# Kernel optimization log

Measured on AMD Instinct MI355X. Metric: run time of the kernel, lower is better.

## Reference

```python
import jax, jax.numpy as jnp
import numpy as np

D_MODEL = 1024
N_HEAD = 16
T = 2048
HEAD = D_MODEL // N_HEAD  # 64
RANKS = [32, 16, 8, 8]
BLOCKS = [2048, 1024, 512, 256]  # seq_len // 2**i ('default')
OFFS = np.cumsum([0] + RANKS)


def setup_inputs() -> dict:
    key = jax.random.key(0)
    k0, k1, k2 = jax.random.split(key, 3)
    s = 0.02
    x = jax.random.normal(k0, (1, T, D_MODEL), dtype=jnp.float32)
    W_attn = jax.random.normal(k1, (D_MODEL, 3 * D_MODEL), dtype=jnp.float32) * s
    b_attn = jnp.zeros((3 * D_MODEL,), dtype=jnp.float32)
    W_proj = jax.random.normal(k2, (D_MODEL, D_MODEL), dtype=jnp.float32) * s
    b_proj = jnp.zeros((D_MODEL,), dtype=jnp.float32)
    return {"x": x, "W_attn": W_attn, "b_attn": b_attn, "W_proj": W_proj, "b_proj": b_proj}


def reference(x, W_attn, b_attn, W_proj, b_proj):
    B = x.shape[0]
    qkv = x @ W_attn + b_attn  # (B,T,3*D)
    q, k, v = jnp.split(qkv, 3, axis=-1)
    # (B,H,T,HEAD)
    q = q.reshape(B, T, N_HEAD, HEAD).transpose(0, 2, 1, 3)
    k = k.reshape(B, T, N_HEAD, HEAD).transpose(0, 2, 1, 3)
    v = v.reshape(B, T, N_HEAD, HEAD).transpose(0, 2, 1, 3)

    att = jnp.zeros((B, N_HEAD, T, T), dtype=x.dtype)
    for i, (bdx, r) in enumerate(zip(BLOCKS, RANKS)):
        nb = T // bdx
        qi = q[..., OFFS[i]:OFFS[i + 1]].reshape(B, N_HEAD, nb, bdx, r)
        ki = k[..., OFFS[i]:OFFS[i + 1]].reshape(B, N_HEAD, nb, bdx, r)
        blk = jnp.einsum('bhnir,bhnjr->bhnij', qi, ki) * (1.0 / r)  # (B,H,nb,bdx,bdx)
        # scatter block-diagonal scores into full T x T matrix
        att5 = att.reshape(B, N_HEAD, nb, bdx, nb, bdx)
        ar = jnp.arange(nb)
        att5 = att5.at[:, :, ar, :, ar, :].add(jnp.moveaxis(blk, 2, 0))
        att = att5.reshape(B, N_HEAD, T, T)

    causal = jnp.tril(jnp.ones((T, T), dtype=bool))
    att = jnp.where(causal, att, -jnp.inf)
    att = jax.nn.softmax(att, axis=-1)
    y = att @ v  # (B,H,T,HEAD)
    y = y.transpose(0, 2, 1, 3).reshape(B, T, D_MODEL)
    return y @ W_proj + b_proj
```

## Files before the change

kernel.cpp:

```cpp
#include <hip/hip_runtime.h>

using bf16x8 = __attribute__((ext_vector_type(8))) short;
using f32x4  = __attribute__((ext_vector_type(4))) float;

#define DEVI __device__ __forceinline__

DEVI unsigned short f2bf(float f) {
  union { float ff; unsigned u; } v; v.ff = f;
  unsigned r = v.u + 0x7FFFu + ((v.u >> 16) & 1u);
  return (unsigned short)(r >> 16);
}

DEVI int cvtpk(float lo, float hi) {
  int r;
  asm("v_cvt_pk_bf16_f32 %0, %1, %2" : "=v"(r) : "v"(lo), "v"(hi));
  return r;
}

DEVI void g2l16(const void* g, void* l) {
  __builtin_amdgcn_global_load_lds(
      (const __attribute__((address_space(1))) unsigned int*)g,
      (__attribute__((address_space(3))) unsigned int*)l, 16, 0, 0);
}

__global__ void k_convx(const float* __restrict__ in, unsigned short* __restrict__ out, int n4) {
  int i = blockIdx.x * 256 + threadIdx.x;
  if (i >= n4) return;
  float4 v = reinterpret_cast<const float4*>(in)[i];
  ushort4 o;
  o.x = f2bf(v.x); o.y = f2bf(v.y); o.z = f2bf(v.z); o.w = f2bf(v.w);
  reinterpret_cast<ushort4*>(out)[i] = o;
}

__global__ void k_tconv(const float* __restrict__ in, unsigned short* __restrict__ out, int R, int C) {
  __shared__ float tile[32][33];
  int c0 = blockIdx.x * 32, r0 = blockIdx.y * 32;
  int x = threadIdx.x, y = threadIdx.y;
  for (int i = y; i < 32; i += 8) tile[i][x] = in[(size_t)(r0 + i) * C + c0 + x];
  __syncthreads();
  for (int i = y; i < 32; i += 8) out[(size_t)(c0 + i) * R + r0 + x] = f2bf(tile[x][i]);
}

__global__ __launch_bounds__(256) void k_gemm_qkv(
    const unsigned short* __restrict__ A, const unsigned short* __restrict__ Bt,
    const float* __restrict__ bias,
    unsigned short* __restrict__ qs, unsigned short* __restrict__ kbuf,
    unsigned short* __restrict__ vT) {
  constexpr int K = 1024;
  __shared__ __align__(16) unsigned short As[2][128 * 64];
  __shared__ __align__(16) unsigned short Bs[2][64 * 64];
  const int lane = threadIdx.x & 63, wid = threadIdx.x >> 6;
  const int m0 = blockIdx.y * 128, n0 = blockIdx.x * 64;
  const int wr = (wid >> 1) * 64, wc = (wid & 1) * 32;
  const int g = lane >> 4, li = lane & 15;
  f32x4 acc[4][2] = {};

#define STAGE_QKV(buf, k0)                                                              \
  {                                                                                     \
    _Pragma("unroll")                                                                   \
    for (int c = wid * 4; c < wid * 4 + 4; c++) {                                       \
      const int flat = c * 1024 + lane * 16;                                            \
      const int row = flat >> 7, colb = flat & 127;                                     \
      g2l16((const char*)A + ((size_t)(m0 + row) * K + (k0)) * 2 + colb,                \
            (char*)As[buf] + c * 1024);                                                 \
    }                                                                                   \
    _Pragma("unroll")                                                                   \
    for (int c = wid * 2; c < wid * 2 + 2; c++) {                                       \
      const int flat = c * 1024 + lane * 16;                                            \
      const int row = flat >> 7, colb = flat & 127;                                     \
      g2l16((const char*)Bt + ((size_t)(n0 + row) * K + (k0)) * 2 + colb,               \
            (char*)Bs[buf] + c * 1024);                                                 \
    }                                                                                   \
  }

  STAGE_QKV(0, 0);
  __syncthreads();
  int buf = 0;
  for (int t = 0; t < 16; t++) {
    if (t < 15) STAGE_QKV(buf ^ 1, (t + 1) * 64);
#pragma unroll
    for (int ks = 0; ks < 2; ks++) {
      const int kk = ks * 32 + g * 8;
      bf16x8 a[4], b[2];
#pragma unroll
      for (int i = 0; i < 4; i++)
        a[i] = *reinterpret_cast<const bf16x8*>(As[buf] + (wr + i * 16 + li) * 64 + kk);
#pragma unroll
      for (int j = 0; j < 2; j++)
        b[j] = *reinterpret_cast<const bf16x8*>(Bs[buf] + (wc + j * 16 + li) * 64 + kk);
#pragma unroll
      for (int i = 0; i < 4; i++)
#pragma unroll
        for (int j = 0; j < 2; j++)
          acc[i][j] = __builtin_amdgcn_mfma_f32_16x16x32_bf16(a[i], b[j], acc[i][j], 0, 0, 0);
    }
    __syncthreads();
    buf ^= 1;
  }

  const int rb = m0 + wr + g * 4;
  const int cb = n0 + wc + li;
#pragma unroll
  for (int j = 0; j < 2; j++) {
    const int c = cb + j * 16;
    const float bv = bias[c];
    const int hq = c >> 6, d = c & 63;
    const float sc = d < 32 ? 0.03125f : (d < 48 ? 0.0625f : 0.125f);
#pragma unroll
    for (int i = 0; i < 4; i++) {
#pragma unroll
      for (int r = 0; r < 4; r++) {
        const int t = rb + i * 16 + r;
        const float val = acc[i][j][r] + bv;
        if (c < 1024) {
          qs[((size_t)(hq * 2048 + t) << 6) + d] = f2bf(val * sc);
        } else if (c < 2048) {
          kbuf[((size_t)((hq - 16) * 2048 + t) << 6) + d] = f2bf(val);
        } else {
          vT[(size_t)((hq - 32) * 64 + d) * 2048 + t] = f2bf(val);
        }
      }
    }
  }
#undef STAGE_QKV
}

DEVI int chunk_off(int qt) {
  const int off[17] = {0,1,2,3,4,6,8,10,12,15,18,21,24,28,32,36,40};
  return off[qt];
}

__global__ __launch_bounds__(256) void k_attn_part(
    const unsigned short* __restrict__ qs, const unsigned short* __restrict__ kbuf,
    const unsigned short* __restrict__ vT,
    float* __restrict__ o_part, float* __restrict__ ml) {
  __shared__ __align__(16) unsigned short Ks[128 * 64];
  __shared__ __align__(16) unsigned short Vs[64 * 128];
  const int lane = threadIdx.x & 63, wid = threadIdx.x >> 6;
  const int g = lane >> 4, li = lane & 15;

  const int h = blockIdx.x / 40;
  const int rem = blockIdx.x % 40;
  int qt = 0;
#pragma unroll
  for (int i = 0; i < 16; i++)
    if (rem >= chunk_off(i + 1)) qt = i + 1;
  const int ci = rem - chunk_off(qt);
  const int kt0 = ci * 4;
  const int kt1 = min(qt, kt0 + 3);
  const int q0 = qt * 128;

  const bf16x8 bzero = {0, 0, 0, 0, 0, 0, 0, 0};

  bf16x8 qf[2][2];
#pragma unroll
  for (int mi = 0; mi < 2; mi++)
#pragma unroll
    for (int ks = 0; ks < 2; ks++) {
      const int t = q0 + wid * 32 + mi * 16 + li;
      const int d = ks * 32 + g * 8;
      qf[mi][ks] = *reinterpret_cast<const bf16x8*>(qs + ((size_t)(h * 2048 + t) << 6) + d);
    }

  f32x4 o[2][4] = {};
  float m_run[2] = {-1e30f, -1e30f}, l_run[2] = {0.f, 0.f};

  const int q256 = qt >> 1;
  for (int kt = kt0; kt <= kt1; kt++) {
    __syncthreads();
    for (int c = wid; c < 16; c += 4) {
      const int fb = c * 1024;
      const int flat = fb + lane * 16;
      {
        const int row = flat >> 7;
        const int cs = (((flat >> 4) & 7) ^ (row & 7)) << 4;
        g2l16((const char*)kbuf + (((size_t)(h * 2048 + kt * 128 + row)) << 7) + cs,
              (char*)Ks + fb);
      }
      {
        const int row = flat >> 8;
        const int cs = (((flat >> 4) & 15) ^ (row & 15)) << 4;
        g2l16((const char*)vT + ((size_t)(h * 64 + row) * 2048 + kt * 128) * 2 + cs,
              (char*)Vs + fb);
      }
    }
    __syncthreads();

    const int x = q256 ^ (kt >> 1);
    const int Keff = (x == 0) ? 64 : ((x >= 4) ? 32 : ((x >= 2) ? 48 : 56));

    f32x4 st[8][2] = {};
#pragma unroll
    for (int cf = 0; cf < 8; cf++) {
      const int krow = cf * 16 + li;
      const bf16x8 a0 = *reinterpret_cast<const bf16x8*>(
          Ks + krow * 64 + ((g ^ (krow & 7)) << 3));
      st[cf][0] = __builtin_amdgcn_mfma_f32_16x16x32_bf16(a0, qf[0][0], st[cf][0], 0, 0, 0);
      st[cf][1] = __builtin_amdgcn_mfma_f32_16x16x32_bf16(a0, qf[1][0], st[cf][1], 0, 0, 0);
    }
    if (Keff > 32) {
      const bool zf = (32 + g * 8) >= Keff;
#pragma unroll
      for (int cf = 0; cf < 8; cf++) {
        const int krow = cf * 16 + li;
        bf16x8 a1 = *reinterpret_cast<const bf16x8*>(
            Ks + krow * 64 + (((4 + g) ^ (krow & 7)) << 3));
        if (zf) a1 = bzero;
        st[cf][0] = __builtin_amdgcn_mfma_f32_16x16x32_bf16(a1, qf[0][1], st[cf][0], 0, 0, 0);
        st[cf][1] = __builtin_amdgcn_mfma_f32_16x16x32_bf16(a1, qf[1][1], st[cf][1], 0, 0, 0);
      }
    }

    if (kt == qt) {
#pragma unroll
      for (int cf = 0; cf < 8; cf++)
#pragma unroll
        for (int mi = 0; mi < 2; mi++)
#pragma unroll
          for (int r = 0; r < 4; r++) {
            const int t2 = cf * 16 + g * 4 + r;
            const int qq = wid * 32 + mi * 16 + li;
            if (t2 > qq) st[cf][mi][r] = -1e30f;
          }
    }

    int pk[2][8][2];
    float corrb[2][4];
#pragma unroll
    for (int mi = 0; mi < 2; mi++) {
      float tm = st[0][mi][0];
#pragma unroll
      for (int cf = 0; cf < 8; cf++)
#pragma unroll
        for (int r = 0; r < 4; r++)
          if (cf | r) tm = fmaxf(tm, st[cf][mi][r]);
      tm = fmaxf(tm, __shfl_xor(tm, 16));
      tm = fmaxf(tm, __shfl_xor(tm, 32));
      const float mn = fmaxf(m_run[mi], tm);
      const float corr = __expf(m_run[mi] - mn);
      m_run[mi] = mn;
      float sum = 0.f;
#pragma unroll
      for (int cf = 0; cf < 8; cf++) {
        const float p0 = __expf(st[cf][mi][0] - mn);
        const float p1 = __expf(st[cf][mi][1] - mn);
        const float p2 = __expf(st[cf][mi][2] - mn);
        const float p3 = __expf(st[cf][mi][3] - mn);
        sum += (p0 + p1) + (p2 + p3);
        pk[mi][cf][0] = cvtpk(p0, p1);
        pk[mi][cf][1] = cvtpk(p2, p3);
      }
      sum += __shfl_xor(sum, 16);
      sum += __shfl_xor(sum, 32);
      l_run[mi] = l_run[mi] * corr + sum;
      corrb[mi][0] = __shfl(corr, 4 * g + 0);
      corrb[mi][1] = __shfl(corr, 4 * g + 1);
      corrb[mi][2] = __shfl(corr, 4 * g + 2);
      corrb[mi][3] = __shfl(corr, 4 * g + 3);
    }
#pragma unroll
    for (int mi = 0; mi < 2; mi++)
#pragma unroll
      for (int nf = 0; nf < 4; nf++)
#pragma unroll
        for (int r = 0; r < 4; r++)
          o[mi][nf][r] *= corrb[mi][r];

#pragma unroll
    for (int ks2 = 0; ks2 < 4; ks2++) {
      bf16x8 pa[2];
#pragma unroll
      for (int mi = 0; mi < 2; mi++) {
        union { int i[4]; bf16x8 v; } u;
        u.i[0] = pk[mi][2 * ks2][0];
        u.i[1] = pk[mi][2 * ks2][1];
        u.i[2] = pk[mi][2 * ks2 + 1][0];
        u.i[3] = pk[mi][2 * ks2 + 1][1];
        pa[mi] = u.v;
      }
      bf16x8 vb[4];
#pragma unroll
      for (int nf = 0; nf < 4; nf++) {
        const int vrow = nf * 16 + li;
        const int rm = vrow & 15;
        const int ch0 = 4 * ks2 + (g >> 1);
        const int b8 = (g & 1) * 8;
        union { struct { int2 lo, hi; } p; bf16x8 v; } u;
        u.p.lo = *reinterpret_cast<const int2*>(
            (const char*)Vs + vrow * 256 + (((ch0 + 0) ^ rm) << 4) + b8);
        u.p.hi = *reinterpret_cast<const int2*>(
            (const char*)Vs + vrow * 256 + (((ch0 + 2) ^ rm) << 4) + b8);
        vb[nf] = u.v;
      }
#pragma unroll
      for (int mi = 0; mi < 2; mi++)
#pragma unroll
        for (int nf = 0; nf < 4; nf++)
          o[mi][nf] = __builtin_amdgcn_mfma_f32_16x16x32_bf16(pa[mi], vb[nf], o[mi][nf], 0, 0, 0);
    }
  }

  const size_t pbase = (size_t)blockIdx.x * 8192;
#pragma unroll
  for (int mi = 0; mi < 2; mi++) {
#pragma unroll
    for (int nf = 0; nf < 4; nf++)
#pragma unroll
      for (int r = 0; r < 4; r++) {
        const int row = wid * 32 + mi * 16 + g * 4 + r;
        o_part[pbase + (size_t)row * 64 + nf * 16 + li] = o[mi][nf][r];
      }
  }
  if (g == 0) {
#pragma unroll
    for (int mi = 0; mi < 2; mi++) {
      const int row = wid * 32 + mi * 16 + li;
      ml[(size_t)blockIdx.x * 256 + row] = m_run[mi];
      ml[(size_t)blockIdx.x * 256 + 128 + row] = l_run[mi];
    }
  }
}

__global__ __launch_bounds__(256) void k_combine(
    const float* __restrict__ o_part, const float* __restrict__ ml,
    unsigned short* __restrict__ yb) {
  const int h = blockIdx.x >> 4, qt = blockIdx.x & 15;
  const int nc = (qt >> 2) + 1;
  const int base = h * 40 + chunk_off(qt);
  const int row = threadIdx.x >> 1;
  const int c0 = (threadIdx.x & 1) * 32;

  float m_i[4], l_i[4];
  float M = -1e30f;
  for (int ci = 0; ci < nc; ci++) {
    m_i[ci] = ml[(size_t)(base + ci) * 256 + row];
    l_i[ci] = ml[(size_t)(base + ci) * 256 + 128 + row];
    M = fmaxf(M, m_i[ci]);
  }
  float L = 0.f, w[4];
  for (int ci = 0; ci < nc; ci++) {
    w[ci] = __expf(m_i[ci] - M);
    L += w[ci] * l_i[ci];
  }
  const float inv = 1.0f / L;

  float acc[32];
#pragma unroll
  for (int j = 0; j < 32; j++) acc[j] = 0.f;
  for (int ci = 0; ci < nc; ci++) {
    const float* src = o_part + (size_t)(base + ci) * 8192 + (size_t)row * 64 + c0;
    const float wc = w[ci];
#pragma unroll
    for (int j4 = 0; j4 < 8; j4++) {
      float4 v = reinterpret_cast<const float4*>(src)[j4];
      acc[j4 * 4 + 0] += wc * v.x;
      acc[j4 * 4 + 1] += wc * v.y;
      acc[j4 * 4 + 2] += wc * v.z;
      acc[j4 * 4 + 3] += wc * v.w;
    }
  }
  const int t = qt * 128 + row;
  unsigned short* dst = yb + (size_t)t * 1024 + h * 64 + c0;
#pragma unroll
  for (int j8 = 0; j8 < 4; j8++) {
    ushort4 pk;
    pk.x = f2bf(acc[j8 * 8 + 0] * inv);
    pk.y = f2bf(acc[j8 * 8 + 1] * inv);
    pk.z = f2bf(acc[j8 * 8 + 2] * inv);
    pk.w = f2bf(acc[j8 * 8 + 3] * inv);
    ushort4 pk2;
    pk2.x = f2bf(acc[j8 * 8 + 4] * inv);
    pk2.y = f2bf(acc[j8 * 8 + 5] * inv);
    pk2.z = f2bf(acc[j8 * 8 + 6] * inv);
    pk2.w = f2bf(acc[j8 * 8 + 7] * inv);
    reinterpret_cast<ushort4*>(dst)[j8 * 2 + 0] = pk;
    reinterpret_cast<ushort4*>(dst)[j8 * 2 + 1] = pk2;
  }
}

__global__ __launch_bounds__(256) void k_gemm_proj(
    const unsigned short* __restrict__ A, const unsigned short* __restrict__ Bt,
    const float* __restrict__ bias, float* __restrict__ out) {
  constexpr int K = 1024;
  __shared__ __align__(16) unsigned short As[2][64 * 64];
  __shared__ __align__(16) unsigned short Bs[2][64 * 64];
  const int lane = threadIdx.x & 63, wid = threadIdx.x >> 6;
  const int m0 = blockIdx.y * 64, n0 = blockIdx.x * 64;
  const int wr = (wid >> 1) * 32, wc = (wid & 1) * 32;
  const int g = lane >> 4, li = lane & 15;
  f32x4 acc[2][2] = {};

#define STAGE_PROJ(buf, k0)                                                             \
  {                                                                                     \
    _Pragma("unroll")                                                                   \
    for (int c = wid * 2; c < wid * 2 + 2; c++) {                                       \
      const int flat = c * 1024 + lane * 16;                                            \
      const int row = flat >> 7, colb = flat & 127;                                     \
      g2l16((const char*)A + ((size_t)(m0 + row) * K + (k0)) * 2 + colb,                \
            (char*)As[buf] + c * 1024);                                                 \
      g2l16((const char*)Bt + ((size_t)(n0 + row) * K + (k0)) * 2 + colb,               \
            (char*)Bs[buf] + c * 1024);                                                 \
    }                                                                                   \
  }

  STAGE_PROJ(0, 0);
  __syncthreads();
  int buf = 0;
  for (int t = 0; t < 16; t++) {
    if (t < 15) STAGE_PROJ(buf ^ 1, (t + 1) * 64);
#pragma unroll
    for (int ks = 0; ks < 2; ks++) {
      const int kk = ks * 32 + g * 8;
      bf16x8 a[2], b[2];
#pragma unroll
      for (int i = 0; i < 2; i++)
        a[i] = *reinterpret_cast<const bf16x8*>(As[buf] + (wr + i * 16 + li) * 64 + kk);
#pragma unroll
      for (int j = 0; j < 2; j++)
        b[j] = *reinterpret_cast<const bf16x8*>(Bs[buf] + (wc + j * 16 + li) * 64 + kk);
#pragma unroll
      for (int i = 0; i < 2; i++)
#pragma unroll
        for (int j = 0; j < 2; j++)
          acc[i][j] = __builtin_amdgcn_mfma_f32_16x16x32_bf16(a[i], b[j], acc[i][j], 0, 0, 0);
    }
    __syncthreads();
    buf ^= 1;
  }

  const int rb = m0 + wr + g * 4;
  const int cb = n0 + wc + li;
#pragma unroll
  for (int j = 0; j < 2; j++) {
    const int c = cb + j * 16;
    const float bv = bias[c];
#pragma unroll
    for (int i = 0; i < 2; i++) {
#pragma unroll
      for (int r = 0; r < 4; r++) {
        const int t = rb + i * 16 + r;
        out[(size_t)t * 1024 + c] = acc[i][j][r] + bv;
      }
    }
  }
#undef STAGE_PROJ
}

extern "C" void kernel_launch(void* const* d_in, const int* in_sizes, int n_in,
                              void* d_out, int out_size, void* d_ws, size_t ws_size,
                              hipStream_t stream) {
  const float* x      = (const float*)d_in[0];
  const float* W_attn = (const float*)d_in[1];
  const float* b_attn = (const float*)d_in[2];
  const float* W_proj = (const float*)d_in[3];
  const float* b_proj = (const float*)d_in[4];
  float* out = (float*)d_out;
  char* ws = (char*)d_ws;
  const size_t MB = 1024 * 1024;
  unsigned short* xb  = (unsigned short*)(ws + 0 * MB);
  unsigned short* WaT = (unsigned short*)(ws + 4 * MB);
  unsigned short* WpT = (unsigned short*)(ws + 10 * MB);
  unsigned short* qs  = (unsigned short*)(ws + 12 * MB);
  unsigned short* kb  = (unsigned short*)(ws + 16 * MB);
  unsigned short* vT  = (unsigned short*)(ws + 20 * MB);
  unsigned short* yb  = (unsigned short*)(ws + 24 * MB);
  float* o_part = (float*)(ws + 28 * MB);
  float* ml     = (float*)(ws + 48 * MB + 256 * 1024);

  k_convx<<<dim3(2048), dim3(256), 0, stream>>>(x, xb, 524288);
  k_tconv<<<dim3(96, 32), dim3(32, 8), 0, stream>>>(W_attn, WaT, 1024, 3072);
  k_tconv<<<dim3(32, 32), dim3(32, 8), 0, stream>>>(W_proj, WpT, 1024, 1024);
  k_gemm_qkv<<<dim3(48, 16), dim3(256), 0, stream>>>(xb, WaT, b_attn, qs, kb, vT);
  k_attn_part<<<dim3(640), dim3(256), 0, stream>>>(qs, kb, vT, o_part, ml);
  k_combine<<<dim3(256), dim3(256), 0, stream>>>(o_part, ml, yb);
  k_gemm_proj<<<dim3(16, 32), dim3(256), 0, stream>>>(yb, WpT, b_proj, out);
}
```

Before: 103.7 us.

## Fuse prep kernels, double-buffer attention KV loads, store partials in bf16

Merges the three conversion/transpose launches into a single k_prep kernel. In the attention-partial kernel, K/V tiles are now double-buffered so the next tile's global-to-LDS load overlaps compute on the current one, and MFMA sections get raised wave priority. The row-max reduction becomes a tree, and partial outputs are stored in bf16 instead of fp32 to halve combine traffic. Costs are doubled LDS use per block, which may lower occupancy, and a small loss of precision in the partial accumulators.

```diff
diff --git a/kernel.cpp b/kernel.cpp
--- a/kernel.cpp
+++ b/kernel.cpp
@@ -1,6 +1,7 @@
 #include <hip/hip_runtime.h>
 
 using bf16x8 = __attribute__((ext_vector_type(8))) short;
+using u16x8  = __attribute__((ext_vector_type(8))) unsigned short;
 using f32x4  = __attribute__((ext_vector_type(4))) float;
 
 #define DEVI __device__ __forceinline__
@@ -11,6 +12,11 @@
   return (unsigned short)(r >> 16);
 }
 
+DEVI float bf2f(unsigned short s) {
+  union { unsigned u; float f; } t; t.u = ((unsigned)s) << 16;
+  return t.f;
+}
+
 DEVI int cvtpk(float lo, float hi) {
   int r;
   asm("v_cvt_pk_bf16_f32 %0, %1, %2" : "=v"(r) : "v"(lo), "v"(hi));
@@ -23,22 +29,37 @@
       (__attribute__((address_space(3))) unsigned int*)l, 16, 0, 0);
 }
 
-__global__ void k_convx(const float* __restrict__ in, unsigned short* __restrict__ out, int n4) {
-  int i = blockIdx.x * 256 + threadIdx.x;
-  if (i >= n4) return;
-  float4 v = reinterpret_cast<const float4*>(in)[i];
-  ushort4 o;
-  o.x = f2bf(v.x); o.y = f2bf(v.y); o.z = f2bf(v.z); o.w = f2bf(v.w);
-  reinterpret_cast<ushort4*>(out)[i] = o;
-}
-
-__global__ void k_tconv(const float* __restrict__ in, unsigned short* __restrict__ out, int R, int C) {
+__global__ __launch_bounds__(256) void k_prep(
+    const float* __restrict__ x, const float* __restrict__ Wa, const float* __restrict__ Wp,
+    unsigned short* __restrict__ xb, unsigned short* __restrict__ WaT,
+    unsigned short* __restrict__ WpT) {
   __shared__ float tile[32][33];
-  int c0 = blockIdx.x * 32, r0 = blockIdx.y * 32;
-  int x = threadIdx.x, y = threadIdx.y;
-  for (int i = y; i < 32; i += 8) tile[i][x] = in[(size_t)(r0 + i) * C + c0 + x];
+  const int b = blockIdx.x;
+  const int tid = threadIdx.x;
+  if (b < 2048) {
+    const int i = b * 256 + tid;
+    float4 v = reinterpret_cast<const float4*>(x)[i];
+    ushort4 o;
+    o.x = f2bf(v.x); o.y = f2bf(v.y); o.z = f2bf(v.z); o.w = f2bf(v.w);
+    reinterpret_cast<ushort4*>(xb)[i] = o;
+    return;
+  }
+  const float* in;
+  unsigned short* out;
+  int c0, r0, C;
+  if (b < 5120) {
+    const int bb = b - 2048;
+    in = Wa; out = WaT; C = 3072;
+    c0 = (bb % 96) * 32; r0 = (bb / 96) * 32;
+  } else {
+    const int bb = b - 5120;
+    in = Wp; out = WpT; C = 1024;
+    c0 = (bb & 31) * 32; r0 = (bb >> 5) * 32;
+  }
+  const int xx = tid & 31, yy = tid >> 5;
+  for (int i = yy; i < 32; i += 8) tile[i][xx] = in[(size_t)(r0 + i) * C + c0 + xx];
   __syncthreads();
-  for (int i = y; i < 32; i += 8) out[(size_t)(c0 + i) * R + r0 + x] = f2bf(tile[x][i]);
+  for (int i = yy; i < 32; i += 8) out[(size_t)(c0 + i) * 1024 + r0 + xx] = f2bf(tile[xx][i]);
 }
 
 __global__ __launch_bounds__(256) void k_gemm_qkv(
@@ -133,9 +154,9 @@
 __global__ __launch_bounds__(256) void k_attn_part(
     const unsigned short* __restrict__ qs, const unsigned short* __restrict__ kbuf,
     const unsigned short* __restrict__ vT,
-    float* __restrict__ o_part, float* __restrict__ ml) {
-  __shared__ __align__(16) unsigned short Ks[128 * 64];
-  __shared__ __align__(16) unsigned short Vs[64 * 128];
+    unsigned short* __restrict__ o_part, float* __restrict__ ml) {
+  __shared__ __align__(16) unsigned short Ks[2][128 * 64];
+  __shared__ __align__(16) unsigned short Vs[2][64 * 128];
   const int lane = threadIdx.x & 63, wid = threadIdx.x >> 6;
   const int g = lane >> 4, li = lane & 15;
 
@@ -152,6 +173,24 @@
 
   const bf16x8 bzero = {0, 0, 0, 0, 0, 0, 0, 0};
 
+#define STAGE_KV(buf, kt)                                                               \
+  for (int c = wid; c < 16; c += 4) {                                                   \
+    const int fb = c * 1024;                                                            \
+    const int flat = fb + lane * 16;                                                    \
+    {                                                                                   \
+      const int row = flat >> 7;                                                        \
+      const int cs = (((flat >> 4) & 7) ^ (row & 7)) << 4;                              \
+      g2l16((const char*)kbuf + (((size_t)(h * 2048 + (kt) * 128 + row)) << 7) + cs,    \
+            (char*)Ks[buf] + fb);                                                       \
+    }                                                                                   \
+    {                                                                                   \
+      const int row = flat >> 8;                                                        \
+      const int cs = (((flat >> 4) & 15) ^ (row & 15)) << 4;                            \
+      g2l16((const char*)vT + ((size_t)(h * 64 + row) * 2048 + (kt) * 128) * 2 + cs,    \
+            (char*)Vs[buf] + fb);                                                       \
+    }                                                                                   \
+  }
+
   bf16x8 qf[2][2];
 #pragma unroll
   for (int mi = 0; mi < 2; mi++)
@@ -166,35 +205,22 @@
   float m_run[2] = {-1e30f, -1e30f}, l_run[2] = {0.f, 0.f};
 
   const int q256 = qt >> 1;
+  STAGE_KV(0, kt0);
+  int buf = 0;
   for (int kt = kt0; kt <= kt1; kt++) {
     __syncthreads();
-    for (int c = wid; c < 16; c += 4) {
-      const int fb = c * 1024;
-      const int flat = fb + lane * 16;
-      {
-        const int row = flat >> 7;
-        const int cs = (((flat >> 4) & 7) ^ (row & 7)) << 4;
-        g2l16((const char*)kbuf + (((size_t)(h * 2048 + kt * 128 + row)) << 7) + cs,
-              (char*)Ks + fb);
-      }
-      {
-        const int row = flat >> 8;
-        const int cs = (((flat >> 4) & 15) ^ (row & 15)) << 4;
-        g2l16((const char*)vT + ((size_t)(h * 64 + row) * 2048 + kt * 128) * 2 + cs,
-              (char*)Vs + fb);
-      }
-    }
-    __syncthreads();
+    if (kt < kt1) STAGE_KV(buf ^ 1, kt + 1);
 
     const int x = q256 ^ (kt >> 1);
     const int Keff = (x == 0) ? 64 : ((x >= 4) ? 32 : ((x >= 2) ? 48 : 56));
 
     f32x4 st[8][2] = {};
+    __builtin_amdgcn_s_setprio(1);
 #pragma unroll
     for (int cf = 0; cf < 8; cf++) {
       const int krow = cf * 16 + li;
       const bf16x8 a0 = *reinterpret_cast<const bf16x8*>(
-          Ks + krow * 64 + ((g ^ (krow & 7)) << 3));
+          Ks[buf] + krow * 64 + ((g ^ (krow & 7)) << 3));
       st[cf][0] = __builtin_amdgcn_mfma_f32_16x16x32_bf16(a0, qf[0][0], st[cf][0], 0, 0, 0);
       st[cf][1] = __builtin_amdgcn_mfma_f32_16x16x32_bf16(a0, qf[1][0], st[cf][1], 0, 0, 0);
     }
@@ -204,12 +230,13 @@
       for (int cf = 0; cf < 8; cf++) {
         const int krow = cf * 16 + li;
         bf16x8 a1 = *reinterpret_cast<const bf16x8*>(
-            Ks + krow * 64 + (((4 + g) ^ (krow & 7)) << 3));
+            Ks[buf] + krow * 64 + (((4 + g) ^ (krow & 7)) << 3));
         if (zf) a1 = bzero;
         st[cf][0] = __builtin_amdgcn_mfma_f32_16x16x32_bf16(a1, qf[0][1], st[cf][0], 0, 0, 0);
         st[cf][1] = __builtin_amdgcn_mfma_f32_16x16x32_bf16(a1, qf[1][1], st[cf][1], 0, 0, 0);
       }
     }
+    __builtin_amdgcn_s_setprio(0);
 
     if (kt == qt) {
 #pragma unroll
@@ -228,12 +255,14 @@
     float corrb[2][4];
 #pragma unroll
     for (int mi = 0; mi < 2; mi++) {
-      float tm = st[0][mi][0];
+      float c4[8];
 #pragma unroll
       for (int cf = 0; cf < 8; cf++)
-#pragma unroll
-        for (int r = 0; r < 4; r++)
-          if (cf | r) tm = fmaxf(tm, st[cf][mi][r]);
+        c4[cf] = fmaxf(fmaxf(st[cf][mi][0], st[cf][mi][1]),
+                       fmaxf(st[cf][mi][2], st[cf][mi][3]));
+      const float ta = fmaxf(fmaxf(c4[0], c4[1]), fmaxf(c4[2], c4[3]));
+      const float tb = fmaxf(fmaxf(c4[4], c4[5]), fmaxf(c4[6], c4[7]));
+      float tm = fmaxf(ta, tb);
       tm = fmaxf(tm, __shfl_xor(tm, 16));
       tm = fmaxf(tm, __shfl_xor(tm, 32));
       const float mn = fmaxf(m_run[mi], tm);
@@ -266,6 +295,7 @@
         for (int r = 0; r < 4; r++)
           o[mi][nf][r] *= corrb[mi][r];
 
+    __builtin_amdgcn_s_setprio(1);
 #pragma unroll
     for (int ks2 = 0; ks2 < 4; ks2++) {
       bf16x8 pa[2];
@@ -287,9 +317,9 @@
         const int b8 = (g & 1) * 8;
         union { struct { int2 lo, hi; } p; bf16x8 v; } u;
         u.p.lo = *reinterpret_cast<const int2*>(
-            (const char*)Vs + vrow * 256 + (((ch0 + 0) ^ rm) << 4) + b8);
+            (const char*)Vs[buf] + vrow * 256 + (((ch0 + 0) ^ rm) << 4) + b8);
         u.p.hi = *reinterpret_cast<const int2*>(
-            (const char*)Vs + vrow * 256 + (((ch0 + 2) ^ rm) << 4) + b8);
+            (const char*)Vs[buf] + vrow * 256 + (((ch0 + 2) ^ rm) << 4) + b8);
         vb[nf] = u.v;
       }
 #pragma unroll
@@ -298,7 +328,10 @@
         for (int nf = 0; nf < 4; nf++)
           o[mi][nf] = __builtin_amdgcn_mfma_f32_16x16x32_bf16(pa[mi], vb[nf], o[mi][nf], 0, 0, 0);
     }
-  }
+    __builtin_amdgcn_s_setprio(0);
+    buf ^= 1;
+  }
+#undef STAGE_KV
 
   const size_t pbase = (size_t)blockIdx.x * 8192;
 #pragma unroll
@@ -308,7 +341,7 @@
 #pragma unroll
       for (int r = 0; r < 4; r++) {
         const int row = wid * 32 + mi * 16 + g * 4 + r;
-        o_part[pbase + (size_t)row * 64 + nf * 16 + li] = o[mi][nf][r];
+        o_part[pbase + (size_t)row * 64 + nf * 16 + li] = f2bf(o[mi][nf][r]);
       }
   }
   if (g == 0) {
@@ -322,7 +355,7 @@
 }
 
 __global__ __launch_bounds__(256) void k_combine(
-    const float* __restrict__ o_part, const float* __restrict__ ml,
+    const unsigned short* __restrict__ o_part, const float* __restrict__ ml,
     unsigned short* __restrict__ yb) {
   const int h = blockIdx.x >> 4, qt = blockIdx.x & 15;
   const int nc = (qt >> 2) + 1;
@@ -348,15 +381,14 @@
 #pragma unroll
   for (int j = 0; j < 32; j++) acc[j] = 0.f;
   for (int ci = 0; ci < nc; ci++) {
-    const float* src = o_part + (size_t)(base + ci) * 8192 + (size_t)row * 64 + c0;
+    const u16x8* src = reinterpret_cast<const u16x8*>(
+        o_part + (size_t)(base + ci) * 8192 + (size_t)row * 64 + c0);
     const float wc = w[ci];
 #pragma unroll
-    for (int j4 = 0; j4 < 8; j4++) {
-      float4 v = reinterpret_cast<const float4*>(src)[j4];
-      acc[j4 * 4 + 0] += wc * v.x;
-      acc[j4 * 4 + 1] += wc * v.y;
-      acc[j4 * 4 + 2] += wc * v.z;
-      acc[j4 * 4 + 3] += wc * v.w;
+    for (int j8 = 0; j8 < 4; j8++) {
+      u16x8 v = src[j8];
+#pragma unroll
+      for (int e = 0; e < 8; e++) acc[j8 * 8 + e] += wc * bf2f(v[e]);
     }
   }
   const int t = qt * 128 + row;
@@ -464,12 +496,10 @@
   unsigned short* kb  = (unsigned short*)(ws + 16 * MB);
   unsigned short* vT  = (unsigned short*)(ws + 20 * MB);
   unsigned short* yb  = (unsigned short*)(ws + 24 * MB);
-  float* o_part = (float*)(ws + 28 * MB);
-  float* ml     = (float*)(ws + 48 * MB + 256 * 1024);
-
-  k_convx<<<dim3(2048), dim3(256), 0, stream>>>(x, xb, 524288);
-  k_tconv<<<dim3(96, 32), dim3(32, 8), 0, stream>>>(W_attn, WaT, 1024, 3072);
-  k_tconv<<<dim3(32, 32), dim3(32, 8), 0, stream>>>(W_proj, WpT, 1024, 1024);
+  unsigned short* o_part = (unsigned short*)(ws + 28 * MB);
+  float* ml     = (float*)(ws + 39 * MB);
+
+  k_prep<<<dim3(6144), dim3(256), 0, stream>>>(x, W_attn, W_proj, xb, WaT, WpT);
   k_gemm_qkv<<<dim3(48, 16), dim3(256), 0, stream>>>(xb, WaT, b_attn, qs, kb, vT);
   k_attn_part<<<dim3(640), dim3(256), 0, stream>>>(qs, kb, vT, o_part, ml);
   k_combine<<<dim3(256), dim3(256), 0, stream>>>(o_part, ml, yb);
```

Measured after the change: 96.52 us. -7.0%, faster.
